# Kernel tuning notes

Hardware: AMD Instinct MI355X
Metric: run time of the kernel (lower is better)

## Reference

```python
import jax, jax.numpy as jnp
import numpy as np

EPS = 1e-5

def binary_activation(x):
    # ReActNet piecewise-polynomial STE: forward = sign(x), grad follows poly
    m1 = (x < -1).astype(x.dtype)
    m2 = (x < 0).astype(x.dtype)
    m3 = (x < 1).astype(x.dtype)
    out1 = -1.0 * m1 + (x * x + 2.0 * x) * (1.0 - m1)
    out2 = out1 * m2 + (-x * x + 2.0 * x) * (1.0 - m2)
    out3 = out2 * m3 + 1.0 * (1.0 - m3)
    return jax.lax.stop_gradient(jnp.sign(x) - out3) + out3

def binary_conv(x, w, stride, padding):
    # per-output-channel scaled sign weights with clamp STE
    scale = jnp.mean(jnp.abs(w), axis=(1, 2, 3), keepdims=True)
    clipped = jnp.clip(w, -1.0, 1.0)
    bw = jax.lax.stop_gradient(scale * jnp.sign(w) - clipped) + clipped
    return jax.lax.conv_general_dilated(
        x, bw, window_strides=(stride, stride),
        padding=[(padding, padding), (padding, padding)],
        dimension_numbers=('NCHW', 'OIHW', 'NCHW'))

def batch_norm(x, g, b):
    mu = jnp.mean(x, axis=(0, 2, 3), keepdims=True)
    var = jnp.mean((x - mu) ** 2, axis=(0, 2, 3), keepdims=True)
    xn = (x - mu) * jax.lax.rsqrt(var + EPS)
    return xn * g[None, :, None, None] + b[None, :, None, None]

def prelu(x, a):
    a = a[None, :, None, None]
    return jnp.where(x >= 0, x, a * x)

def setup_inputs() -> dict:
    key = jax.random.key(0)
    ks = jax.random.split(key, 12)
    N, C, H, W = 32, 256, 56, 56
    d = {
        'x': jax.random.normal(ks[0], (N, C, H, W), jnp.float32),
        'b11': jax.random.normal(ks[1], (1, C, 1, 1), jnp.float32) * 0.1,
        'b12': jax.random.normal(ks[2], (1, C, 1, 1), jnp.float32) * 0.1,
        'b13': jax.random.normal(ks[3], (1, C, 1, 1), jnp.float32) * 0.1,
        'b21': jax.random.normal(ks[4], (1, C, 1, 1), jnp.float32) * 0.1,
        'b22': jax.random.normal(ks[5], (1, C, 1, 1), jnp.float32) * 0.1,
        'b23': jax.random.normal(ks[6], (1, C, 1, 1), jnp.float32) * 0.1,
        'w3x3': jax.random.normal(ks[7], (C, C, 3, 3), jnp.float32) * 0.05,
        'wpw': jax.random.normal(ks[8], (C, C, 1, 1), jnp.float32) * 0.05,
        'g1': jnp.ones((C,), jnp.float32),
        'be1': jnp.zeros((C,), jnp.float32),
        'g2': jnp.ones((C,), jnp.float32),
        'be2': jnp.zeros((C,), jnp.float32),
        'p1': jnp.full((C,), 0.25, jnp.float32),
        'p2': jnp.full((C,), 0.25, jnp.float32),
    }
    return d

def reference(x, b11, b12, b13, b21, b22, b23, w3x3, wpw, g1, be1, g2, be2, p1, p2):
    # stride=1, inplanes == planes branch
    out1 = binary_activation(x + b11)
    out1 = binary_conv(out1, w3x3, stride=1, padding=1)
    out1 = batch_norm(out1, g1, be1)
    out1 = x + out1
    out1 = prelu(out1 + b12, p1) + b13
    out2 = binary_activation(out1 + b21)
    out2 = binary_conv(out2, wpw, stride=1, padding=0)
    out2 = batch_norm(out2, g2, be2)
    out2 = out2 + out1
    out2 = prelu(out2 + b22, p2) + b23
    return out2
```

## Files before the change

kernel.cpp:

```cpp
#include <hip/hip_runtime.h>

typedef __attribute__((ext_vector_type(4))) float  f32x4;
typedef __attribute__((ext_vector_type(4))) short  s16x4;
typedef __attribute__((ext_vector_type(4))) int    i32x4;

#define MFMAI8(a, b, c) __builtin_amdgcn_mfma_i32_16x16x64_i8((a), (b), (c), 0, 0, 0)

__device__ __forceinline__ void gload_lds16(const void* g, void* l) {
  __builtin_amdgcn_global_load_lds((const __attribute__((address_space(1))) void*)g,
                                   (__attribute__((address_space(3))) void*)l, 16, 0, 0);
}

__device__ __forceinline__ char sgn8(float v) {
  return v > 0.f ? (char)1 : (v < 0.f ? (char)-1 : (char)0);
}

__global__ __launch_bounds__(256) void prep_w(const float* __restrict__ w3,
                                              const float* __restrict__ wpw,
                                              char* __restrict__ w1s,
                                              char* __restrict__ w2s,
                                              float* __restrict__ scale1,
                                              float* __restrict__ scale2) {
  const int o = blockIdx.x;
  const int t = threadIdx.x;
  float s = 0.f;
  if (blockIdx.y == 0) {
    for (int u = t; u < 2304; u += 256) {
      int i = u / 9, tap = u % 9;
      float v = w3[(size_t)(o * 256 + i) * 9 + tap];
      s += fabsf(v);
      w1s[(size_t)(tap * 256 + o) * 256 + i] = sgn8(v);
    }
  } else {
    float v = wpw[o * 256 + t];
    s = fabsf(v);
    w2s[o * 256 + t] = sgn8(v);
  }
  for (int m = 1; m < 64; m <<= 1) s += __shfl_xor(s, m);
  __shared__ float red[4];
  if ((t & 63) == 0) red[t >> 6] = s;
  __syncthreads();
  if (t == 0) {
    float tot = red[0] + red[1] + red[2] + red[3];
    if (blockIdx.y == 0) scale1[o] = tot / 2304.f;
    else                 scale2[o] = tot / 256.f;
  }
}

__global__ __launch_bounds__(256) void sign_nhwc(const float* __restrict__ x,
                                                 const float* __restrict__ b11,
                                                 char* __restrict__ out) {
  __shared__ unsigned short l[56 * 128];
  __shared__ float cB[256];
  const int h = blockIdx.x, n = blockIdx.y, t = threadIdx.x;
  cB[t] = b11[t];
  __syncthreads();
  const int wv = t & 15, cg = t >> 4;
  if (wv < 14) {
    const int w0 = wv * 4;
    const int swz = (wv & 7) << 3;
#pragma unroll 4
    for (int it = 0; it < 8; ++it) {
      int cp = it * 16 + cg;
      int c0 = cp * 2;
      size_t i0 = (size_t)(n * 256 + c0) * 3136 + h * 56 + w0;
      f32x4 x0 = *(const f32x4*)(x + i0);
      f32x4 x1 = *(const f32x4*)(x + i0 + 3136);
      float bb0 = cB[c0], bb1 = cB[c0 + 1];
      int cs = cp ^ swz;
#pragma unroll
      for (int j = 0; j < 4; ++j) {
        unsigned short pk = (unsigned char)sgn8(x0[j] + bb0) |
                            ((unsigned short)(unsigned char)sgn8(x1[j] + bb1) << 8);
        l[(w0 + j) * 128 + cs] = pk;
      }
    }
  }
  __syncthreads();
  char* op = out + ((size_t)(n * 56 + h) * 56) * 256;
  for (int u = t; u < 56 * 16; u += 256) {
    int w2 = u >> 4, cp = u & 15;
    *(i32x4*)(op + w2 * 256 + cp * 16) =
        *(const i32x4*)&l[w2 * 128 + ((cp * 8) ^ (((w2 >> 2) & 7) << 3))];
  }
}

__global__ __launch_bounds__(256, 2) void conv3x3(const char* __restrict__ sIn,
                                                  const char* __restrict__ wSgn,
                                                  short* __restrict__ raw,
                                                  float* __restrict__ S,
                                                  float* __restrict__ SS) {
  __shared__ char lin[2][10 * 58 * 64];

  int bid = (blockIdx.x & 7) * 112 + (blockIdx.x >> 3);
  const int ot = bid & 3;
  const int g  = bid >> 2;
  const int ht = g % 7, n = g / 7;
  const int h0 = ht * 8, oc0 = ot * 64;

  const int t = threadIdx.x;
  const int lane = t & 63, wv = t >> 6;
  const int cl = lane & 15, kk = lane >> 4;

  {
    i32x4* pl = (i32x4*)&lin[0][0];
    for (int u = t; u < 2 * 10 * 58 * 4; u += 256) pl[u] = (i32x4){0, 0, 0, 0};
  }
  __syncthreads();

  const int pw = t >> 2, sl = t & 3;
  const int srcslot = sl ^ (((1 + pw) >> 1) & 3);

#define STAGE_3x3(icc, bi)                                                          \
  {                                                                                 \
    if (t < 224) {                                                                  \
      _Pragma("unroll")                                                             \
      for (int rr = 0; rr < 10; ++rr) {                                             \
        int h = h0 - 1 + rr;                                                        \
        char* dst = &lin[bi][(rr * 58 + 1 + pw) * 64 + sl * 16];                    \
        if (h >= 0 && h < 56) {                                                     \
          const char* src = sIn +                                                   \
              ((size_t)((n * 56 + h) * 56 + pw) * 256 + (icc) * 64 + srcslot * 16); \
          gload_lds16(src, dst);                                                    \
        } else {                                                                    \
          *(i32x4*)dst = (i32x4){0, 0, 0, 0};                                       \
        }                                                                           \
      }                                                                             \
    }                                                                               \
  }

  int r0[7], c0[7];
#pragma unroll
  for (int nf = 0; nf < 7; ++nf) {
    int p = wv * 112 + nf * 16 + cl;
    r0[nf] = p / 56;
    c0[nf] = p % 56;
  }

  i32x4 acc[4][7];
#pragma unroll
  for (int m = 0; m < 4; ++m)
#pragma unroll
    for (int nf = 0; nf < 7; ++nf) acc[m][nf] = (i32x4){0, 0, 0, 0};

  STAGE_3x3(0, 0);
  __syncthreads();

  for (int icc = 0; icc < 4; ++icc) {
    const int cur = icc & 1;
    if (icc < 3) STAGE_3x3(icc + 1, cur ^ 1);

#pragma unroll
    for (int kh = 0; kh < 3; ++kh)
#pragma unroll
      for (int kw = 0; kw < 3; ++kw) {
        const int tap = kh * 3 + kw;
        i32x4 a[4];
#pragma unroll
        for (int m = 0; m < 4; ++m)
          a[m] = *(const i32x4*)(wSgn +
              (((size_t)(tap * 256 + oc0 + m * 16 + cl)) << 8) + icc * 64 + kk * 16);
#pragma unroll
        for (int nf = 0; nf < 7; ++nf) {
          int col = c0[nf] + kw;
          int addr = ((r0[nf] + kh) * 58 + col) * 64 + ((kk ^ ((col >> 1) & 3)) << 4);
          i32x4 b = *(const i32x4*)(&lin[cur][addr]);
#pragma unroll
          for (int m = 0; m < 4; ++m) acc[m][nf] = MFMAI8(a[m], b, acc[m][nf]);
        }
      }
    __syncthreads();
  }

#pragma unroll
  for (int m = 0; m < 4; ++m) {
    float sm[4] = {0.f, 0.f, 0.f, 0.f}, sq[4] = {0.f, 0.f, 0.f, 0.f};
#pragma unroll
    for (int nf = 0; nf < 7; ++nf) {
      int p = wv * 112 + nf * 16 + cl;
      int h = h0 + p / 56, w = p % 56;
      size_t base = ((size_t)n * 256 + oc0 + m * 16 + kk * 4) * 3136 + h * 56 + w;
      i32x4 v = acc[m][nf];
#pragma unroll
      for (int r2 = 0; r2 < 4; ++r2) {
        raw[base + (size_t)r2 * 3136] = (short)v[r2];
        float fv = (float)v[r2];
        sm[r2] += fv;
        sq[r2] += fv * fv;
      }
    }
#pragma unroll
    for (int r2 = 0; r2 < 4; ++r2) {
      float aa = sm[r2], qq = sq[r2];
      aa += __shfl_xor(aa, 1); qq += __shfl_xor(qq, 1);
      aa += __shfl_xor(aa, 2); qq += __shfl_xor(qq, 2);
      aa += __shfl_xor(aa, 4); qq += __shfl_xor(qq, 4);
      aa += __shfl_xor(aa, 8); qq += __shfl_xor(qq, 8);
      if (cl == 0) {
        int oc = oc0 + m * 16 + kk * 4 + r2;
        atomicAdd(&S[oc], aa);
        atomicAdd(&SS[oc], qq);
      }
    }
  }
}

__global__ __launch_bounds__(256, 2) void conv1x1(const char* __restrict__ sIn,
                                                  const char* __restrict__ wSgn,
                                                  short* __restrict__ raw,
                                                  float* __restrict__ S,
                                                  float* __restrict__ SS) {
  __shared__ char lin[112 * 256];

  const int b = blockIdx.x;
  const int n = b / 28;
  const int hw0 = (b % 28) * 112;
  const size_t px0 = (size_t)n * 3136 + hw0;
  const int t = threadIdx.x, lane = t & 63, wv = t >> 6;
  const int cl = lane & 15, kk = lane >> 4;

#pragma unroll
  for (int i = 0; i < 7; ++i) {
    int u = i * 256 + t;
    int px = u >> 4, s = u & 15;
    const char* src = sIn + (px0 + px) * 256 + ((s ^ (px & 7)) * 16);
    gload_lds16(src, lin + u * 16);
  }

  i32x4 acc[4][7];
#pragma unroll
  for (int m = 0; m < 4; ++m)
#pragma unroll
    for (int nf = 0; nf < 7; ++nf) acc[m][nf] = (i32x4){0, 0, 0, 0};

  __syncthreads();

#pragma unroll
  for (int icc = 0; icc < 4; ++icc) {
    i32x4 bfr[7];
#pragma unroll
    for (int nf = 0; nf < 7; ++nf) {
      int px = nf * 16 + cl;
      int srd = (icc * 4 + kk) ^ (px & 7);
      bfr[nf] = *(const i32x4*)(lin + px * 256 + srd * 16);
    }
#pragma unroll
    for (int m = 0; m < 4; ++m) {
      i32x4 a = *(const i32x4*)(wSgn +
          (((size_t)(wv * 64 + m * 16 + cl)) << 8) + icc * 64 + kk * 16);
#pragma unroll
      for (int nf = 0; nf < 7; ++nf) acc[m][nf] = MFMAI8(a, bfr[nf], acc[m][nf]);
    }
  }

#pragma unroll
  for (int m = 0; m < 4; ++m) {
    float sm[4] = {0.f, 0.f, 0.f, 0.f}, sq[4] = {0.f, 0.f, 0.f, 0.f};
    size_t base0 = ((size_t)n * 256 + wv * 64 + m * 16 + kk * 4) * 3136 + hw0;
#pragma unroll
    for (int nf = 0; nf < 7; ++nf) {
      i32x4 v = acc[m][nf];
#pragma unroll
      for (int r2 = 0; r2 < 4; ++r2) {
        raw[base0 + (size_t)r2 * 3136 + nf * 16 + cl] = (short)v[r2];
        float fv = (float)v[r2];
        sm[r2] += fv;
        sq[r2] += fv * fv;
      }
    }
#pragma unroll
    for (int r2 = 0; r2 < 4; ++r2) {
      float aa = sm[r2], qq = sq[r2];
      aa += __shfl_xor(aa, 1); qq += __shfl_xor(qq, 1);
      aa += __shfl_xor(aa, 2); qq += __shfl_xor(qq, 2);
      aa += __shfl_xor(aa, 4); qq += __shfl_xor(qq, 4);
      aa += __shfl_xor(aa, 8); qq += __shfl_xor(qq, 8);
      if (cl == 0) {
        int oc = wv * 64 + m * 16 + kk * 4 + r2;
        atomicAdd(&S[oc], aa);
        atomicAdd(&SS[oc], qq);
      }
    }
  }
}

__global__ void bn_coef(const float* __restrict__ S, const float* __restrict__ SS,
                        const float* __restrict__ scale, const float* __restrict__ g,
                        const float* __restrict__ be, const float* __restrict__ bext,
                        float* __restrict__ A, float* __restrict__ B) {
  int o = threadIdx.x;
  const float invN = 1.f / 100352.f;
  float mu_r  = S[o] * invN;
  float var_r = SS[o] * invN - mu_r * mu_r;
  float sc    = scale[o];
  float rstd  = rsqrtf(sc * sc * var_r + 1e-5f);
  A[o] = g[o] * rstd * sc;
  B[o] = be[o] - g[o] * rstd * sc * mu_r + bext[o];
}

__global__ __launch_bounds__(256) void mid_fuse(const short* __restrict__ raw,
                                                const float* __restrict__ x,
                                                const float* __restrict__ A1,
                                                const float* __restrict__ B1,
                                                const float* __restrict__ p1,
                                                const float* __restrict__ b13,
                                                const float* __restrict__ b21,
                                                float* __restrict__ t1,
                                                char* __restrict__ s2) {
  __shared__ unsigned short l[56 * 128];
  __shared__ float cA[256], cB[256], cP[256], cD[256], cE[256];
  const int h = blockIdx.x, n = blockIdx.y, t = threadIdx.x;
  cA[t] = A1[t]; cB[t] = B1[t]; cP[t] = p1[t]; cD[t] = b13[t]; cE[t] = b21[t];
  __syncthreads();
  const int wv = t & 15, cg = t >> 4;
  if (wv < 14) {
    const int w0 = wv * 4;
    const int swz = (wv & 7) << 3;
#pragma unroll 2
    for (int it = 0; it < 8; ++it) {
      int cp = it * 16 + cg;
      int c0 = cp * 2;
      size_t i0 = (size_t)(n * 256 + c0) * 3136 + h * 56 + w0;
      f32x4 x0 = *(const f32x4*)(x + i0);
      f32x4 x1 = *(const f32x4*)(x + i0 + 3136);
      s16x4 r0 = *(const s16x4*)(raw + i0);
      s16x4 r1 = *(const s16x4*)(raw + i0 + 3136);
      float a0 = cA[c0], b0 = cB[c0], p0 = cP[c0], d0 = cD[c0], e0 = cE[c0];
      float a1 = cA[c0+1], b1 = cB[c0+1], p1v = cP[c0+1], d1 = cD[c0+1], e1 = cE[c0+1];
      f32x4 o0, o1;
      int cs = cp ^ swz;
#pragma unroll
      for (int j = 0; j < 4; ++j) {
        float u0 = x0[j] + a0 * (float)r0[j] + b0;
        u0 = (u0 >= 0.f ? u0 : p0 * u0) + d0;
        o0[j] = u0;
        float u1 = x1[j] + a1 * (float)r1[j] + b1;
        u1 = (u1 >= 0.f ? u1 : p1v * u1) + d1;
        o1[j] = u1;
        unsigned short pk = (unsigned char)sgn8(u0 + e0) |
                            ((unsigned short)(unsigned char)sgn8(u1 + e1) << 8);
        l[(w0 + j) * 128 + cs] = pk;
      }
      *(f32x4*)(t1 + i0) = o0;
      *(f32x4*)(t1 + i0 + 3136) = o1;
    }
  }
  __syncthreads();
  char* op = s2 + ((size_t)(n * 56 + h) * 56) * 256;
  for (int u = t; u < 56 * 16; u += 256) {
    int w2 = u >> 4, cp = u & 15;
    *(i32x4*)(op + w2 * 256 + cp * 16) =
        *(const i32x4*)&l[w2 * 128 + ((cp * 8) ^ (((w2 >> 2) & 7) << 3))];
  }
}

__global__ __launch_bounds__(256) void final_fuse(const short* __restrict__ raw,
                                                  const float* __restrict__ A2,
                                                  const float* __restrict__ B2,
                                                  const float* __restrict__ p2,
                                                  const float* __restrict__ b23,
                                                  float* out) {
  const int c = blockIdx.x & 255;
  const size_t base = (size_t)blockIdx.x * 3136;
  const float a = A2[c], b = B2[c], p = p2[c], d = b23[c];
  for (int i = threadIdx.x; i < 784; i += 256) {
    s16x4 r  = *(const s16x4*)(raw + base + (size_t)i * 4);
    f32x4 tt = *(const f32x4*)(out + base + (size_t)i * 4);
    f32x4 o;
#pragma unroll
    for (int j = 0; j < 4; ++j) {
      float v = a * (float)r[j] + b + tt[j];
      o[j] = (v >= 0.f ? v : p * v) + d;
    }
    *(f32x4*)(out + base + (size_t)i * 4) = o;
  }
}

extern "C" void kernel_launch(void* const* d_in, const int* in_sizes, int n_in,
                              void* d_out, int out_size, void* d_ws, size_t ws_size,
                              hipStream_t stream) {
  const float* x   = (const float*)d_in[0];
  const float* b11 = (const float*)d_in[1];
  const float* b12 = (const float*)d_in[2];
  const float* b13 = (const float*)d_in[3];
  const float* b21 = (const float*)d_in[4];
  const float* b22 = (const float*)d_in[5];
  const float* b23 = (const float*)d_in[6];
  const float* w3  = (const float*)d_in[7];
  const float* wpw = (const float*)d_in[8];
  const float* g1  = (const float*)d_in[9];
  const float* be1 = (const float*)d_in[10];
  const float* g2  = (const float*)d_in[11];
  const float* be2 = (const float*)d_in[12];
  const float* p1  = (const float*)d_in[13];
  const float* p2  = (const float*)d_in[14];

  char* ws = (char*)d_ws;
  short* raw    = (short*)(ws);
  char*  sgn    = (char*)(ws + 51380224);
  char*  w1s    = (char*)(ws + 77070336);
  char*  w2s    = (char*)(ws + 77660160);
  float* scale1 = (float*)(ws + 77725696);
  float* scale2 = (float*)(ws + 77726720);
  float* S1     = (float*)(ws + 77727744);
  float* SS1    = (float*)(ws + 77728768);
  float* S2     = (float*)(ws + 77729792);
  float* SS2    = (float*)(ws + 77730816);
  float* A1     = (float*)(ws + 77731840);
  float* B1     = (float*)(ws + 77732864);
  float* A2     = (float*)(ws + 77733888);
  float* B2     = (float*)(ws + 77734912);
  float* t1     = (float*)d_out;

  hipMemsetAsync(ws + 77727744, 0, 4096, stream);

  prep_w<<<dim3(256, 2), 256, 0, stream>>>(w3, wpw, w1s, w2s, scale1, scale2);
  sign_nhwc<<<dim3(56, 32), 256, 0, stream>>>(x, b11, sgn);
  conv3x3<<<dim3(896), 256, 0, stream>>>(sgn, w1s, raw, S1, SS1);
  bn_coef<<<1, 256, 0, stream>>>(S1, SS1, scale1, g1, be1, b12, A1, B1);
  mid_fuse<<<dim3(56, 32), 256, 0, stream>>>(raw, x, A1, B1, p1, b13, b21, t1, sgn);
  conv1x1<<<dim3(896), 256, 0, stream>>>(sgn, w2s, raw, S2, SS2);
  bn_coef<<<1, 256, 0, stream>>>(S2, SS2, scale2, g2, be2, b22, A2, B2);
  final_fuse<<<dim3(8192), 256, 0, stream>>>(raw, A2, B2, p2, b23, (float*)d_out);
}
```

Baseline: 416.1 us.

## Stage conv weights in LDS and coalesce raw output stores via LDS transpose

The 3x3 conv now loads each input-channel chunk of the input tile and weights into registers ahead of the compute, then writes them to single-buffered LDS after the MFMA loop, replacing the async global-to-LDS double buffer. The A operand is read from swizzled LDS instead of directly from global memory. Both conv kernels transpose their int16 results through LDS so the raw output is written as 16-byte coalesced stores rather than scattered 2-byte stores. In exchange there are extra barriers per chunk and per output group, and more register pressure from holding the prefetch in registers.

```diff
diff --git a/kernel.cpp b/kernel.cpp
--- a/kernel.cpp
+++ b/kernel.cpp
@@ -90,7 +90,8 @@
                                                   short* __restrict__ raw,
                                                   float* __restrict__ S,
                                                   float* __restrict__ SS) {
-  __shared__ char lin[2][10 * 58 * 64];
+  __shared__ char lin[10 * 58 * 64];
+  __shared__ char lw[9 * 64 * 64];
 
   int bid = (blockIdx.x & 7) * 112 + (blockIdx.x >> 3);
   const int ot = bid & 3;
@@ -102,31 +103,50 @@
   const int lane = t & 63, wv = t >> 6;
   const int cl = lane & 15, kk = lane >> 4;
 
-  {
-    i32x4* pl = (i32x4*)&lin[0][0];
-    for (int u = t; u < 2 * 10 * 58 * 4; u += 256) pl[u] = (i32x4){0, 0, 0, 0};
-  }
-  __syncthreads();
-
   const int pw = t >> 2, sl = t & 3;
   const int srcslot = sl ^ (((1 + pw) >> 1) & 3);
 
-#define STAGE_3x3(icc, bi)                                                          \
-  {                                                                                 \
-    if (t < 224) {                                                                  \
-      _Pragma("unroll")                                                             \
-      for (int rr = 0; rr < 10; ++rr) {                                             \
-        int h = h0 - 1 + rr;                                                        \
-        char* dst = &lin[bi][(rr * 58 + 1 + pw) * 64 + sl * 16];                    \
-        if (h >= 0 && h < 56) {                                                     \
-          const char* src = sIn +                                                   \
-              ((size_t)((n * 56 + h) * 56 + pw) * 256 + (icc) * 64 + srcslot * 16); \
-          gload_lds16(src, dst);                                                    \
-        } else {                                                                    \
-          *(i32x4*)dst = (i32x4){0, 0, 0, 0};                                       \
-        }                                                                           \
-      }                                                                             \
-    }                                                                               \
+  if (t < 80) {
+    int rr = t >> 3, q = t & 7;
+    int col = (q >> 2) ? 57 : 0;
+    *(i32x4*)&lin[(rr * 58 + col) * 64 + (q & 3) * 16] = (i32x4){0, 0, 0, 0};
+  }
+
+  i32x4 inreg[10], wreg[9];
+
+#define LOADR(icc)                                                               \
+  {                                                                              \
+    if (t < 224) {                                                               \
+      _Pragma("unroll")                                                          \
+      for (int rr = 0; rr < 10; ++rr) {                                          \
+        int h = h0 - 1 + rr;                                                     \
+        if (h >= 0 && h < 56)                                                    \
+          inreg[rr] = *(const i32x4*)(sIn +                                      \
+              ((size_t)((n * 56 + h) * 56 + pw) * 256 + (icc) * 64 + srcslot * 16)); \
+        else                                                                     \
+          inreg[rr] = (i32x4){0, 0, 0, 0};                                       \
+      }                                                                          \
+    }                                                                            \
+    _Pragma("unroll")                                                            \
+    for (int i = 0; i < 9; ++i) {                                                \
+      int u = i * 256 + t;                                                       \
+      int tap = u >> 8, oc_e = (u >> 2) & 63;                                    \
+      int wslot = (u & 3) ^ ((u >> 3) & 3);                                      \
+      wreg[i] = *(const i32x4*)(wSgn +                                           \
+          ((size_t)(tap * 256 + oc0 + oc_e) * 256 + (icc) * 64 + wslot * 16));   \
+    }                                                                            \
+  }
+
+#define WRITER()                                                                 \
+  {                                                                              \
+    if (t < 224) {                                                               \
+      _Pragma("unroll")                                                          \
+      for (int rr = 0; rr < 10; ++rr)                                            \
+        *(i32x4*)&lin[(rr * 58 + 1 + pw) * 64 + sl * 16] = inreg[rr];            \
+    }                                                                            \
+    _Pragma("unroll")                                                            \
+    for (int i = 0; i < 9; ++i)                                                  \
+      *(i32x4*)&lw[(i * 256 + t) * 16] = wreg[i];                                \
   }
 
   int r0[7], c0[7];
@@ -143,12 +163,12 @@
 #pragma unroll
     for (int nf = 0; nf < 7; ++nf) acc[m][nf] = (i32x4){0, 0, 0, 0};
 
-  STAGE_3x3(0, 0);
+  LOADR(0);
+  WRITER();
   __syncthreads();
 
   for (int icc = 0; icc < 4; ++icc) {
-    const int cur = icc & 1;
-    if (icc < 3) STAGE_3x3(icc + 1, cur ^ 1);
+    if (icc < 3) LOADR(icc + 1);
 
 #pragma unroll
     for (int kh = 0; kh < 3; ++kh)
@@ -158,32 +178,34 @@
         i32x4 a[4];
 #pragma unroll
         for (int m = 0; m < 4; ++m)
-          a[m] = *(const i32x4*)(wSgn +
-              (((size_t)(tap * 256 + oc0 + m * 16 + cl)) << 8) + icc * 64 + kk * 16);
+          a[m] = *(const i32x4*)(&lw[(tap * 64 + m * 16 + cl) * 64 +
+                                     ((kk ^ ((cl >> 1) & 3)) << 4)]);
 #pragma unroll
         for (int nf = 0; nf < 7; ++nf) {
           int col = c0[nf] + kw;
           int addr = ((r0[nf] + kh) * 58 + col) * 64 + ((kk ^ ((col >> 1) & 3)) << 4);
-          i32x4 b = *(const i32x4*)(&lin[cur][addr]);
+          i32x4 b = *(const i32x4*)(&lin[addr]);
 #pragma unroll
           for (int m = 0; m < 4; ++m) acc[m][nf] = MFMAI8(a[m], b, acc[m][nf]);
         }
       }
     __syncthreads();
-  }
-
+    if (icc < 3) {
+      WRITER();
+      __syncthreads();
+    }
+  }
+
+  unsigned short* tb = (unsigned short*)lin;
+  const size_t ocbase = (size_t)n * 256 + oc0;
 #pragma unroll
   for (int m = 0; m < 4; ++m) {
     float sm[4] = {0.f, 0.f, 0.f, 0.f}, sq[4] = {0.f, 0.f, 0.f, 0.f};
 #pragma unroll
     for (int nf = 0; nf < 7; ++nf) {
-      int p = wv * 112 + nf * 16 + cl;
-      int h = h0 + p / 56, w = p % 56;
-      size_t base = ((size_t)n * 256 + oc0 + m * 16 + kk * 4) * 3136 + h * 56 + w;
       i32x4 v = acc[m][nf];
 #pragma unroll
       for (int r2 = 0; r2 < 4; ++r2) {
-        raw[base + (size_t)r2 * 3136] = (short)v[r2];
         float fv = (float)v[r2];
         sm[r2] += fv;
         sq[r2] += fv * fv;
@@ -202,6 +224,22 @@
         atomicAdd(&SS[oc], qq);
       }
     }
+    __syncthreads();
+#pragma unroll
+    for (int nf = 0; nf < 7; ++nf) {
+      i32x4 v = acc[m][nf];
+      int px = wv * 112 + nf * 16 + cl;
+#pragma unroll
+      for (int r2 = 0; r2 < 4; ++r2)
+        tb[(kk * 4 + r2) * 472 + px] = (unsigned short)(short)v[r2];
+    }
+    __syncthreads();
+    for (int u = t; u < 896; u += 256) {
+      int qc = u >> 6, r = u & 63, ocl = r >> 2, c3 = r & 3;
+      int c8 = qc * 4 + c3;
+      *(i32x4*)(raw + (ocbase + m * 16 + ocl) * 3136 + h0 * 56 + c8 * 8) =
+          *(const i32x4*)&tb[ocl * 472 + c8 * 8];
+    }
   }
 }
 
@@ -253,16 +291,16 @@
     }
   }
 
+  __syncthreads();
+  unsigned short* tb = (unsigned short*)lin;
 #pragma unroll
   for (int m = 0; m < 4; ++m) {
     float sm[4] = {0.f, 0.f, 0.f, 0.f}, sq[4] = {0.f, 0.f, 0.f, 0.f};
-    size_t base0 = ((size_t)n * 256 + wv * 64 + m * 16 + kk * 4) * 3136 + hw0;
 #pragma unroll
     for (int nf = 0; nf < 7; ++nf) {
       i32x4 v = acc[m][nf];
 #pragma unroll
       for (int r2 = 0; r2 < 4; ++r2) {
-        raw[base0 + (size_t)r2 * 3136 + nf * 16 + cl] = (short)v[r2];
         float fv = (float)v[r2];
         sm[r2] += fv;
         sq[r2] += fv * fv;
@@ -279,6 +317,26 @@
         int oc = wv * 64 + m * 16 + kk * 4 + r2;
         atomicAdd(&S[oc], aa);
         atomicAdd(&SS[oc], qq);
+      }
+    }
+    __syncthreads();
+#pragma unroll
+    for (int nf = 0; nf < 7; ++nf) {
+      i32x4 v = acc[m][nf];
+      int px = nf * 16 + cl;
+#pragma unroll
+      for (int r2 = 0; r2 < 4; ++r2)
+        tb[(wv * 16 + kk * 4 + r2) * 120 + px] = (unsigned short)(short)v[r2];
+    }
+    __syncthreads();
+#pragma unroll
+    for (int i = 0; i < 4; ++i) {
+      int u = i * 256 + t;
+      int ocg = u >> 4, c8 = u & 15;
+      if (c8 < 14) {
+        int oc = (ocg >> 4) * 64 + m * 16 + (ocg & 15);
+        *(i32x4*)(raw + ((size_t)n * 256 + oc) * 3136 + hw0 + c8 * 8) =
+            *(const i32x4*)&tb[ocg * 120 + c8 * 8];
       }
     }
   }
```

After: 452.3 us. 8.7% more time.

## Stage conv outputs through LDS for coalesced stores; use integer BN statistics

Applied to the files above, without the earlier changes.

Both conv kernels now transpose their int16 accumulator tiles through shared memory and write them back as 16-byte coalesced rows, replacing scattered 2-byte stores. BN sum and sum-of-squares are accumulated as integers and reduced with 64-bit atomics, and bn_coef works in double precision. The 3x3 conv also prefetches weights two taps ahead in registers, and it zeroes only the halo columns of the LDS tile instead of clearing the whole buffer. The exchange adds extra __syncthreads per output group and 64-bit atomics, and it needs a larger workspace for the statistics.

```diff
diff --git a/kernel.cpp b/kernel.cpp
--- a/kernel.cpp
+++ b/kernel.cpp
@@ -88,8 +88,8 @@
 __global__ __launch_bounds__(256, 2) void conv3x3(const char* __restrict__ sIn,
                                                   const char* __restrict__ wSgn,
                                                   short* __restrict__ raw,
-                                                  float* __restrict__ S,
-                                                  float* __restrict__ SS) {
+                                                  long long* __restrict__ S,
+                                                  long long* __restrict__ SS) {
   __shared__ char lin[2][10 * 58 * 64];
 
   int bid = (blockIdx.x & 7) * 112 + (blockIdx.x >> 3);
@@ -102,9 +102,11 @@
   const int lane = t & 63, wv = t >> 6;
   const int cl = lane & 15, kk = lane >> 4;
 
-  {
-    i32x4* pl = (i32x4*)&lin[0][0];
-    for (int u = t; u < 2 * 10 * 58 * 4; u += 256) pl[u] = (i32x4){0, 0, 0, 0};
+  if (t < 160) {
+    int bi = t / 80, r = t % 80;
+    int rr = r >> 3, q = r & 7;
+    int col = (q >> 2) ? 57 : 0;
+    *(i32x4*)&lin[bi][(rr * 58 + col) * 64 + (q & 3) * 16] = (i32x4){0, 0, 0, 0};
   }
   __syncthreads();
 
@@ -129,6 +131,14 @@
     }                                                                               \
   }
 
+  const char* wbase = wSgn + ((size_t)(oc0 + cl) << 8) + kk * 16;
+#define WLOAD(dst, tap, icc)                                                        \
+  {                                                                                 \
+    _Pragma("unroll")                                                               \
+    for (int m_ = 0; m_ < 4; ++m_)                                                  \
+      dst[m_] = *(const i32x4*)(wbase + (size_t)(tap) * 65536 + m_ * 4096 + (icc) * 64); \
+  }
+
   int r0[7], c0[7];
 #pragma unroll
   for (int nf = 0; nf < 7; ++nf) {
@@ -146,61 +156,77 @@
   STAGE_3x3(0, 0);
   __syncthreads();
 
+  i32x4 wA[4], wB[4];
   for (int icc = 0; icc < 4; ++icc) {
     const int cur = icc & 1;
+    WLOAD(wA, 0, icc);
+    WLOAD(wB, 1, icc);
     if (icc < 3) STAGE_3x3(icc + 1, cur ^ 1);
 
 #pragma unroll
-    for (int kh = 0; kh < 3; ++kh)
-#pragma unroll
-      for (int kw = 0; kw < 3; ++kw) {
-        const int tap = kh * 3 + kw;
-        i32x4 a[4];
-#pragma unroll
-        for (int m = 0; m < 4; ++m)
-          a[m] = *(const i32x4*)(wSgn +
-              (((size_t)(tap * 256 + oc0 + m * 16 + cl)) << 8) + icc * 64 + kk * 16);
-#pragma unroll
-        for (int nf = 0; nf < 7; ++nf) {
-          int col = c0[nf] + kw;
-          int addr = ((r0[nf] + kh) * 58 + col) * 64 + ((kk ^ ((col >> 1) & 3)) << 4);
-          i32x4 b = *(const i32x4*)(&lin[cur][addr]);
-#pragma unroll
-          for (int m = 0; m < 4; ++m) acc[m][nf] = MFMAI8(a[m], b, acc[m][nf]);
-        }
-      }
+    for (int tap = 0; tap < 9; ++tap) {
+      i32x4 w0 = wA[0], w1 = wA[1], w2 = wA[2], w3 = wA[3];
+      wA[0] = wB[0]; wA[1] = wB[1]; wA[2] = wB[2]; wA[3] = wB[3];
+      if (tap < 7) WLOAD(wB, tap + 2, icc);
+      const int kh = tap / 3, kw = tap % 3;
+#pragma unroll
+      for (int nf = 0; nf < 7; ++nf) {
+        int col = c0[nf] + kw;
+        int addr = ((r0[nf] + kh) * 58 + col) * 64 + ((kk ^ ((col >> 1) & 3)) << 4);
+        i32x4 b = *(const i32x4*)(&lin[cur][addr]);
+        acc[0][nf] = MFMAI8(w0, b, acc[0][nf]);
+        acc[1][nf] = MFMAI8(w1, b, acc[1][nf]);
+        acc[2][nf] = MFMAI8(w2, b, acc[2][nf]);
+        acc[3][nf] = MFMAI8(w3, b, acc[3][nf]);
+      }
+    }
     __syncthreads();
   }
 
+  unsigned short* tb = (unsigned short*)&lin[0][0];
+  const size_t ocbase = (size_t)n * 256 + oc0;
 #pragma unroll
   for (int m = 0; m < 4; ++m) {
-    float sm[4] = {0.f, 0.f, 0.f, 0.f}, sq[4] = {0.f, 0.f, 0.f, 0.f};
+    int sm[4] = {0, 0, 0, 0};
+    unsigned sq[4] = {0, 0, 0, 0};
 #pragma unroll
     for (int nf = 0; nf < 7; ++nf) {
-      int p = wv * 112 + nf * 16 + cl;
-      int h = h0 + p / 56, w = p % 56;
-      size_t base = ((size_t)n * 256 + oc0 + m * 16 + kk * 4) * 3136 + h * 56 + w;
       i32x4 v = acc[m][nf];
 #pragma unroll
       for (int r2 = 0; r2 < 4; ++r2) {
-        raw[base + (size_t)r2 * 3136] = (short)v[r2];
-        float fv = (float)v[r2];
-        sm[r2] += fv;
-        sq[r2] += fv * fv;
+        sm[r2] += v[r2];
+        sq[r2] += (unsigned)(v[r2] * v[r2]);
       }
     }
 #pragma unroll
     for (int r2 = 0; r2 < 4; ++r2) {
-      float aa = sm[r2], qq = sq[r2];
+      int aa = sm[r2];
+      unsigned qq = sq[r2];
       aa += __shfl_xor(aa, 1); qq += __shfl_xor(qq, 1);
       aa += __shfl_xor(aa, 2); qq += __shfl_xor(qq, 2);
       aa += __shfl_xor(aa, 4); qq += __shfl_xor(qq, 4);
       aa += __shfl_xor(aa, 8); qq += __shfl_xor(qq, 8);
       if (cl == 0) {
         int oc = oc0 + m * 16 + kk * 4 + r2;
-        atomicAdd(&S[oc], aa);
-        atomicAdd(&SS[oc], qq);
-      }
+        atomicAdd((unsigned long long*)&S[oc], (unsigned long long)(long long)aa);
+        atomicAdd((unsigned long long*)&SS[oc], (unsigned long long)qq);
+      }
+    }
+    __syncthreads();
+#pragma unroll
+    for (int nf = 0; nf < 7; ++nf) {
+      i32x4 v = acc[m][nf];
+      int px = wv * 112 + nf * 16 + cl;
+#pragma unroll
+      for (int r2 = 0; r2 < 4; ++r2)
+        tb[(kk * 4 + r2) * 472 + px] = (unsigned short)(short)v[r2];
+    }
+    __syncthreads();
+    for (int u = t; u < 896; u += 256) {
+      int qc = u >> 6, r = u & 63, ocl = r >> 2, c3 = r & 3;
+      int c8 = qc * 4 + c3;
+      *(i32x4*)(raw + (ocbase + m * 16 + ocl) * 3136 + h0 * 56 + c8 * 8) =
+          *(const i32x4*)&tb[ocl * 472 + c8 * 8];
     }
   }
 }
@@ -208,8 +234,8 @@
 __global__ __launch_bounds__(256, 2) void conv1x1(const char* __restrict__ sIn,
                                                   const char* __restrict__ wSgn,
                                                   short* __restrict__ raw,
-                                                  float* __restrict__ S,
-                                                  float* __restrict__ SS) {
+                                                  long long* __restrict__ S,
+                                                  long long* __restrict__ SS) {
   __shared__ char lin[112 * 256];
 
   const int b = blockIdx.x;
@@ -253,49 +279,71 @@
     }
   }
 
+  __syncthreads();
+  unsigned short* tb = (unsigned short*)lin;
 #pragma unroll
   for (int m = 0; m < 4; ++m) {
-    float sm[4] = {0.f, 0.f, 0.f, 0.f}, sq[4] = {0.f, 0.f, 0.f, 0.f};
-    size_t base0 = ((size_t)n * 256 + wv * 64 + m * 16 + kk * 4) * 3136 + hw0;
+    int sm[4] = {0, 0, 0, 0};
+    unsigned sq[4] = {0, 0, 0, 0};
 #pragma unroll
     for (int nf = 0; nf < 7; ++nf) {
       i32x4 v = acc[m][nf];
 #pragma unroll
       for (int r2 = 0; r2 < 4; ++r2) {
-        raw[base0 + (size_t)r2 * 3136 + nf * 16 + cl] = (short)v[r2];
-        float fv = (float)v[r2];
-        sm[r2] += fv;
-        sq[r2] += fv * fv;
+        sm[r2] += v[r2];
+        sq[r2] += (unsigned)(v[r2] * v[r2]);
       }
     }
 #pragma unroll
     for (int r2 = 0; r2 < 4; ++r2) {
-      float aa = sm[r2], qq = sq[r2];
+      int aa = sm[r2];
+      unsigned qq = sq[r2];
       aa += __shfl_xor(aa, 1); qq += __shfl_xor(qq, 1);
       aa += __shfl_xor(aa, 2); qq += __shfl_xor(qq, 2);
       aa += __shfl_xor(aa, 4); qq += __shfl_xor(qq, 4);
       aa += __shfl_xor(aa, 8); qq += __shfl_xor(qq, 8);
       if (cl == 0) {
         int oc = wv * 64 + m * 16 + kk * 4 + r2;
-        atomicAdd(&S[oc], aa);
-        atomicAdd(&SS[oc], qq);
-      }
-    }
-  }
-}
-
-__global__ void bn_coef(const float* __restrict__ S, const float* __restrict__ SS,
+        atomicAdd((unsigned long long*)&S[oc], (unsigned long long)(long long)aa);
+        atomicAdd((unsigned long long*)&SS[oc], (unsigned long long)qq);
+      }
+    }
+    __syncthreads();
+#pragma unroll
+    for (int nf = 0; nf < 7; ++nf) {
+      i32x4 v = acc[m][nf];
+      int px = nf * 16 + cl;
+#pragma unroll
+      for (int r2 = 0; r2 < 4; ++r2)
+        tb[(wv * 16 + kk * 4 + r2) * 120 + px] = (unsigned short)(short)v[r2];
+    }
+    __syncthreads();
+#pragma unroll
+    for (int i = 0; i < 4; ++i) {
+      int u = i * 256 + t;
+      int ocg = u >> 4, c8 = u & 15;
+      if (c8 < 14) {
+        int oc = (ocg >> 4) * 64 + m * 16 + (ocg & 15);
+        *(i32x4*)(raw + ((size_t)n * 256 + oc) * 3136 + hw0 + c8 * 8) =
+            *(const i32x4*)&tb[ocg * 120 + c8 * 8];
+      }
+    }
+  }
+}
+
+__global__ void bn_coef(const long long* __restrict__ S, const long long* __restrict__ SS,
                         const float* __restrict__ scale, const float* __restrict__ g,
                         const float* __restrict__ be, const float* __restrict__ bext,
                         float* __restrict__ A, float* __restrict__ B) {
   int o = threadIdx.x;
-  const float invN = 1.f / 100352.f;
-  float mu_r  = S[o] * invN;
-  float var_r = SS[o] * invN - mu_r * mu_r;
-  float sc    = scale[o];
-  float rstd  = rsqrtf(sc * sc * var_r + 1e-5f);
-  A[o] = g[o] * rstd * sc;
-  B[o] = be[o] - g[o] * rstd * sc * mu_r + bext[o];
+  const double invN = 1.0 / 100352.0;
+  double mu_r  = (double)S[o] * invN;
+  double var_r = (double)SS[o] * invN - mu_r * mu_r;
+  double sc    = (double)scale[o];
+  double rstd  = 1.0 / sqrt(sc * sc * var_r + 1e-5);
+  double a     = (double)g[o] * rstd * sc;
+  A[o] = (float)a;
+  B[o] = (float)((double)be[o] - a * mu_r + (double)bext[o]);
 }
 
 __global__ __launch_bounds__(256) void mid_fuse(const short* __restrict__ raw,
@@ -396,23 +444,23 @@
   const float* p2  = (const float*)d_in[14];
 
   char* ws = (char*)d_ws;
-  short* raw    = (short*)(ws);
-  char*  sgn    = (char*)(ws + 51380224);
-  char*  w1s    = (char*)(ws + 77070336);
-  char*  w2s    = (char*)(ws + 77660160);
-  float* scale1 = (float*)(ws + 77725696);
-  float* scale2 = (float*)(ws + 77726720);
-  float* S1     = (float*)(ws + 77727744);
-  float* SS1    = (float*)(ws + 77728768);
-  float* S2     = (float*)(ws + 77729792);
-  float* SS2    = (float*)(ws + 77730816);
-  float* A1     = (float*)(ws + 77731840);
-  float* B1     = (float*)(ws + 77732864);
-  float* A2     = (float*)(ws + 77733888);
-  float* B2     = (float*)(ws + 77734912);
-  float* t1     = (float*)d_out;
-
-  hipMemsetAsync(ws + 77727744, 0, 4096, stream);
+  short*      raw    = (short*)(ws);
+  char*       sgn    = (char*)(ws + 51380224);
+  char*       w1s    = (char*)(ws + 77070336);
+  char*       w2s    = (char*)(ws + 77660160);
+  float*      scale1 = (float*)(ws + 77725696);
+  float*      scale2 = (float*)(ws + 77726720);
+  long long*  S1     = (long long*)(ws + 77727744);
+  long long*  SS1    = (long long*)(ws + 77729792);
+  long long*  S2     = (long long*)(ws + 77731840);
+  long long*  SS2    = (long long*)(ws + 77733888);
+  float*      A1     = (float*)(ws + 77735936);
+  float*      B1     = (float*)(ws + 77736960);
+  float*      A2     = (float*)(ws + 77737984);
+  float*      B2     = (float*)(ws + 77739008);
+  float*      t1     = (float*)d_out;
+
+  hipMemsetAsync(ws + 77727744, 0, 8192, stream);
 
   prep_w<<<dim3(256, 2), 256, 0, stream>>>(w3, wpw, w1s, w2s, scale1, scale2);
   sign_nhwc<<<dim3(56, 32), 256, 0, stream>>>(x, b11, sgn);
```

Measured after the change: 435.2 us. +4.6%, slower.
